# Optimization experiments

Hardware: AMD Instinct MI355X
Metric: run time of the kernel (lower is better)

The kernel has to match this reference:

```python
import jax, jax.numpy as jnp
import numpy as np

BETA = 0.25


def setup_inputs() -> dict:
    key = jax.random.key(0)
    k1, k2 = jax.random.split(key)
    B, C, H, W = 32, 64, 64, 64
    K = 1024
    z = jax.random.normal(k1, (B, C, H, W), dtype=jnp.float32)
    # nn.Embedding init: uniform(-1/K, 1/K)
    embedding = jax.random.uniform(k2, (K, C), dtype=jnp.float32,
                                   minval=-1.0 / K, maxval=1.0 / K)
    return {"z": z, "embedding": embedding}


def reference(z, embedding):
    B, C, H, W = z.shape
    z_hw_c = jnp.transpose(z, (0, 2, 3, 1))            # [B,H,W,C]
    z_flat = z_hw_c.reshape(-1, C)                      # [N,C], N=B*H*W
    # squared L2 distance: ||z||^2 + ||e||^2 - 2 z e^T
    d = (jnp.sum(z_flat ** 2, axis=1, keepdims=True)
         + jnp.sum(embedding ** 2, axis=1)
         - 2.0 * jnp.matmul(z_flat, embedding.T))       # [N,K]
    idx = jnp.argmin(d, axis=1)                         # [N]
    z_q = embedding[idx].reshape(z_hw_c.shape)          # [B,H,W,C]
    # commitment + codebook loss (detach emulated with stop_gradient)
    loss = (jnp.mean((jax.lax.stop_gradient(z_q) - z_hw_c) ** 2)
            + BETA * jnp.mean((z_q - jax.lax.stop_gradient(z_hw_c)) ** 2))
    # straight-through estimator
    z_q_st = z_hw_c + jax.lax.stop_gradient(z_q - z_hw_c)
    z_q_out = jnp.transpose(z_q_st, (0, 3, 1, 2))       # [B,C,H,W]
    min_encoding_indices = idx.reshape(B, H, W)
    return z_q_out, min_encoding_indices, loss
```

## Files before the change

### kernel.cpp

```cpp
#include <hip/hip_runtime.h>

#define C 64
#define K 1024
#define HW 4096
#define N_TOTAL 131072
#define OUT0 8388608
#define MT 128
#define KT 64
#define NTILES (K / KT)

#define WS_EK        0
#define WS_PARTIALS  1024
#define WS_ETG       3072
#define WS_NEED_FLOATS (3072 + C * K)

typedef unsigned int u32;
typedef unsigned long long u64;

__device__ __forceinline__ u64 packdk(float d, int k) {
    u32 b = __float_as_uint(d);
    u32 m = b ^ ((u32)((int)b >> 31) | 0x80000000u);
    return ((u64)m << 32) | (u32)k;
}

__global__ __launch_bounds__(256) void eprep_kernel(const float* __restrict__ E,
                                                    float* __restrict__ Etg,
                                                    float* __restrict__ ek) {
#pragma clang fp contract(off)
    int k = blockIdx.x * 256 + threadIdx.x;
    const float* e = E + k * C;
    float ev[C];
#pragma unroll
    for (int c4 = 0; c4 < 16; ++c4) {
        float4 v = *(const float4*)(e + c4 * 4);
        ev[c4 * 4 + 0] = v.x; ev[c4 * 4 + 1] = v.y;
        ev[c4 * 4 + 2] = v.z; ev[c4 * 4 + 3] = v.w;
    }
    float r[8];
#pragma unroll
    for (int j = 0; j < 8; ++j) r[j] = ev[j] * ev[j];
#pragma unroll
    for (int i = 8; i < C; i += 8)
#pragma unroll
        for (int j = 0; j < 8; ++j) r[j] += ev[i + j] * ev[i + j];
    ek[k] = ((r[0] + r[1]) + (r[2] + r[3])) + ((r[4] + r[5]) + (r[6] + r[7]));
#pragma unroll
    for (int c = 0; c < C; ++c) Etg[c * K + k] = ev[c];
}

__global__ __launch_bounds__(256, 2) void vq_main(const float* __restrict__ Z,
                                                  const float* __restrict__ E,
                                                  const float* __restrict__ Etg,
                                                  const float* __restrict__ ek,
                                                  float* __restrict__ out,
                                                  float* __restrict__ partials) {
#pragma clang fp contract(off)
    __shared__ float Zt[C * MT];
    __shared__ float EtS[C * KT];
    __shared__ float znbuf[MT];
    __shared__ u64 red[4][8][8];

    const int t = threadIdx.x;
    const int n0 = blockIdx.x * MT;
    const int b = n0 >> 12;
    const int hw0 = n0 & 4095;
    const float* zbase = Z + b * (C * HW) + hw0;

#pragma unroll
    for (int r = 0; r < 8; ++r) {
        int idx4 = r * 256 + t;
        int c = idx4 >> 5, n4 = idx4 & 31;
        float4 v = *(const float4*)(zbase + c * HW + n4 * 4);
        *(float4*)(&Zt[c * MT + n4 * 4]) = v;
    }
    __syncthreads();

    if (t < MT) {
        float r8[8];
#pragma unroll
        for (int j = 0; j < 8; ++j) { float v = Zt[j * MT + t]; r8[j] = v * v; }
#pragma unroll
        for (int i = 1; i < 8; ++i)
#pragma unroll
            for (int j = 0; j < 8; ++j) { float v = Zt[(i * 8 + j) * MT + t]; r8[j] += v * v; }
        znbuf[t] = ((r8[0] + r8[1]) + (r8[2] + r8[3])) + ((r8[4] + r8[5]) + (r8[6] + r8[7]));
    }
    __syncthreads();

    const int wave = t >> 6, lane = t & 63;
    const int i_l = lane & 7, j_l = lane >> 3;
    const int ig = ((wave & 1) << 3) | i_l;
    const int jg = ((wave >> 1) << 3) | j_l;

    float znm[8];
#pragma unroll
    for (int m = 0; m < 8; ++m) znm[m] = znbuf[ig * 8 + m];

    float dmin[8];
    int qb[8];
#pragma unroll
    for (int m = 0; m < 8; ++m) { dmin[m] = __builtin_inff(); qb[m] = 0; }

#pragma unroll 1
    for (int tile = 0; tile < NTILES; ++tile) {
        __syncthreads();
#pragma unroll
        for (int p = 0; p < 4; ++p) {
            int idx = p * 256 + t;
            int c = idx >> 4, kk = idx & 15;
            float4 v = *(const float4*)(Etg + c * K + tile * KT + kk * 4);
            *(float4*)(&EtS[c * KT + kk * 4]) = v;
        }
        __syncthreads();

        float4 ekv = *(const float4*)(ek + tile * KT + jg * 4);
        float ekq[4] = {ekv.x, ekv.y, ekv.z, ekv.w};

        float acc[8][4];
#pragma unroll
        for (int m = 0; m < 8; ++m)
#pragma unroll
            for (int q = 0; q < 4; ++q) acc[m][q] = 0.0f;

#pragma unroll 4
        for (int c = 0; c < C; ++c) {
            float4 za = *(const float4*)(&Zt[c * MT + ig * 8]);
            float4 zb = *(const float4*)(&Zt[c * MT + ig * 8 + 4]);
            float4 ea = *(const float4*)(&EtS[c * KT + jg * 4]);
            float zm[8] = {za.x, za.y, za.z, za.w, zb.x, zb.y, zb.z, zb.w};
            float eq[4] = {ea.x, ea.y, ea.z, ea.w};
#pragma unroll
            for (int m = 0; m < 8; ++m)
#pragma unroll
                for (int q = 0; q < 4; ++q)
                    acc[m][q] = __builtin_fmaf(zm[m], eq[q], acc[m][q]);
        }

        const int qbase = tile * 4;
#pragma unroll
        for (int m = 0; m < 8; ++m)
#pragma unroll
            for (int q = 0; q < 4; ++q) {
                float A = znm[m] + ekq[q];
                float d = __builtin_fmaf(-2.0f, acc[m][q], A);
                if (d < dmin[m]) { dmin[m] = d; qb[m] = qbase + q; }
            }
    }

    u64 bestp[8];
#pragma unroll
    for (int m = 0; m < 8; ++m) {
        int q4 = qb[m];
        int k = (q4 >> 2) * KT + jg * 4 + (q4 & 3);
        bestp[m] = packdk(dmin[m], k);
    }
#pragma unroll
    for (int m = 0; m < 8; ++m) {
        u64 v = bestp[m];
#pragma unroll
        for (int mask = 8; mask <= 32; mask <<= 1) {
            u64 o = __shfl_xor(v, mask, 64);
            v = o < v ? o : v;
        }
        bestp[m] = v;
    }
    if (j_l == 0) {
#pragma unroll
        for (int m = 0; m < 8; ++m) red[wave][i_l][m] = bestp[m];
    }
    __syncthreads();

    if (t < MT) {
        int igg = t >> 3, m = t & 7;
        int ihalf = igg >> 3, iw = igg & 7;
        u64 a = red[ihalf][iw][m];
        u64 b2 = red[ihalf + 2][iw][m];
        u64 v = b2 < a ? b2 : a;
        int best = (int)(v & 0xFFFFFFFFu);
        int n = n0 + t;
        out[OUT0 + n] = (float)best;

        const float4* eb4 = (const float4*)(E + best * C);
        float* o0 = out + b * (C * HW) + hw0 + t;
        float ls = 0.0f;
#pragma unroll
        for (int c4 = 0; c4 < 16; ++c4) {
            float4 e4 = eb4[c4];
            int cb = c4 * 4;
            float z0 = Zt[(cb + 0) * MT + t], z1 = Zt[(cb + 1) * MT + t];
            float z2 = Zt[(cb + 2) * MT + t], z3 = Zt[(cb + 3) * MT + t];
            float f0 = e4.x - z0; o0[(cb + 0) * HW] = z0 + f0; ls += f0 * f0;
            float f1 = e4.y - z1; o0[(cb + 1) * HW] = z1 + f1; ls += f1 * f1;
            float f2 = e4.z - z2; o0[(cb + 2) * HW] = z2 + f2; ls += f2 * f2;
            float f3 = e4.w - z3; o0[(cb + 3) * HW] = z3 + f3; ls += f3 * f3;
        }
#pragma unroll
        for (int off = 32; off > 0; off >>= 1) ls += __shfl_xor(ls, off, 64);
        if ((t & 63) == 0) partials[n >> 6] = ls;
    }
}

__global__ __launch_bounds__(256) void ek_kernel(const float* __restrict__ E,
                                                 float* __restrict__ ek) {
#pragma clang fp contract(off)
    int k = blockIdx.x * 256 + threadIdx.x;
    if (k >= K) return;
    const float* e = E + k * C;
    float r[8];
#pragma unroll
    for (int j = 0; j < 8; ++j) { float v = e[j]; r[j] = v * v; }
#pragma unroll
    for (int i = 8; i < C; i += 8) {
#pragma unroll
        for (int j = 0; j < 8; ++j) { float v = e[i + j]; r[j] += v * v; }
    }
    ek[k] = ((r[0] + r[1]) + (r[2] + r[3])) + ((r[4] + r[5]) + (r[6] + r[7]));
}

__global__ __launch_bounds__(256, 4) void vq_combined(const float* __restrict__ Z,
                                                      const float* __restrict__ E,
                                                      const float* __restrict__ ek,
                                                      float* __restrict__ out,
                                                      float* __restrict__ partials) {
#pragma clang fp contract(off)
    int n = blockIdx.x * 256 + threadIdx.x;
    int b = n >> 12;
    int hw = n & 4095;
    const float* zp = Z + b * (C * HW) + hw;

    float z[C];
#pragma unroll
    for (int c = 0; c < C; ++c) z[c] = zp[c * HW];
    float zn;
    {
        float r[8];
#pragma unroll
        for (int j = 0; j < 8; ++j) r[j] = z[j] * z[j];
#pragma unroll
        for (int i = 8; i < C; i += 8) {
#pragma unroll
            for (int j = 0; j < 8; ++j) r[j] += z[i + j] * z[i + j];
        }
        zn = ((r[0] + r[1]) + (r[2] + r[3])) + ((r[4] + r[5]) + (r[6] + r[7]));
    }

    float dmin = __builtin_inff();
    int best = 0;
#pragma unroll 1
    for (int k = 0; k < K; k += 4) {
        const float* e0 = E + k * C;
        float a0 = 0.0f, a1 = 0.0f, a2 = 0.0f, a3 = 0.0f;
#pragma unroll
        for (int c = 0; c < C; ++c) {
            float zc = z[c];
            a0 = __builtin_fmaf(zc, e0[c], a0);
            a1 = __builtin_fmaf(zc, e0[C + c], a1);
            a2 = __builtin_fmaf(zc, e0[2 * C + c], a2);
            a3 = __builtin_fmaf(zc, e0[3 * C + c], a3);
        }
        float A0 = zn + ek[k],     A1 = zn + ek[k + 1];
        float A2 = zn + ek[k + 2], A3 = zn + ek[k + 3];
        float d0 = A0 - 2.0f * a0, d1 = A1 - 2.0f * a1;
        float d2 = A2 - 2.0f * a2, d3 = A3 - 2.0f * a3;
        if (d0 < dmin) { dmin = d0; best = k; }
        if (d1 < dmin) { dmin = d1; best = k + 1; }
        if (d2 < dmin) { dmin = d2; best = k + 2; }
        if (d3 < dmin) { dmin = d3; best = k + 3; }
    }

    const float4* eb4 = (const float4*)(E + best * C);
    float* o0 = out + b * (C * HW) + hw;
    float ls = 0.0f;
#pragma unroll
    for (int c4 = 0; c4 < 16; ++c4) {
        float4 e4 = eb4[c4];
        int cb = c4 * 4;
        float f0 = e4.x - z[cb + 0]; o0[(cb + 0) * HW] = z[cb + 0] + f0; ls += f0 * f0;
        float f1 = e4.y - z[cb + 1]; o0[(cb + 1) * HW] = z[cb + 1] + f1; ls += f1 * f1;
        float f2 = e4.z - z[cb + 2]; o0[(cb + 2) * HW] = z[cb + 2] + f2; ls += f2 * f2;
        float f3 = e4.w - z[cb + 3]; o0[(cb + 3) * HW] = z[cb + 3] + f3; ls += f3 * f3;
    }
    out[OUT0 + n] = (float)best;
#pragma unroll
    for (int off = 32; off > 0; off >>= 1) ls += __shfl_xor(ls, off, 64);
    if ((threadIdx.x & 63) == 0) partials[n >> 6] = ls;
}

__global__ __launch_bounds__(256) void loss_kernel(const float* __restrict__ partials,
                                                   float* __restrict__ out) {
    __shared__ double sm[256];
    int t = threadIdx.x;
    double s = 0.0;
    for (int i = t; i < (N_TOTAL / 64); i += 256) s += (double)partials[i];
    sm[t] = s;
    __syncthreads();
    for (int o = 128; o > 0; o >>= 1) {
        if (t < o) sm[t] += sm[t + o];
        __syncthreads();
    }
    if (t == 0) {
        float m = (float)(sm[0] * (1.0 / 8388608.0));
        float loss = m + 0.25f * m;
        out[OUT0 + N_TOTAL] = loss;
    }
}

extern "C" void kernel_launch(void* const* d_in, const int* in_sizes, int n_in,
                              void* d_out, int out_size, void* d_ws, size_t ws_size,
                              hipStream_t stream) {
    const float* Z = (const float*)d_in[0];
    const float* E = (const float*)d_in[1];
    float* out = (float*)d_out;
    float* ws = (float*)d_ws;
    float* ek = ws + WS_EK;
    float* partials = ws + WS_PARTIALS;

    if (ws_size >= (size_t)WS_NEED_FLOATS * sizeof(float)) {
        float* Etg = ws + WS_ETG;
        hipLaunchKernelGGL(eprep_kernel, dim3(K / 256), dim3(256), 0, stream,
                           E, Etg, ek);
        hipLaunchKernelGGL(vq_main, dim3(N_TOTAL / MT), dim3(256), 0, stream,
                           Z, E, Etg, ek, out, partials);
    } else {
        hipLaunchKernelGGL(ek_kernel, dim3(4), dim3(256), 0, stream, E, ek);
        hipLaunchKernelGGL(vq_combined, dim3(N_TOTAL / 256), dim3(256), 0, stream,
                           Z, E, ek, out, partials);
    }
    hipLaunchKernelGGL(loss_kernel, dim3(1), dim3(256), 0, stream, partials, out);
}
```

Measured before the change: 234.4 us.

## Compute VQ distances with split-bf16 MFMA plus exact fp32 fallback for ambiguous rows

Replaces the scalar fp32 FMA distance GEMM with bf16 hi/lo split MFMA (3-term product) over a pre-swizzled bf16 codebook loaded to LDS via global_load_lds. Each row tracks best and second-best distance; rows with a small gap (or a failed spot check against an fp32 dot) are appended to a list and recomputed exactly in fp32 by a fallback kernel. The epilogue and loss are split into separate kernels. The intent is to move the dominant matmul onto matrix cores, at the cost of extra launches, a second pass over Z, and atomics.

```diff
diff --git a/kernel.cpp b/kernel.cpp
--- a/kernel.cpp
+++ b/kernel.cpp
@@ -6,27 +6,47 @@
 #define N_TOTAL 131072
 #define OUT0 8388608
 #define MT 128
-#define KT 64
-#define NTILES (K / KT)
+#define KT2 64
+#define NT2 (K / KT2)
+
+#define GAP_THR 2.5e-4f
+#define CHK_THR 1e-4f
 
 #define WS_EK        0
-#define WS_PARTIALS  1024
-#define WS_ETG       3072
-#define WS_NEED_FLOATS (3072 + C * K)
+#define WS_ROWLOSS   1024
+#define WS_BESTI     132096
+#define WS_ULIST     263168
+#define WS_UCOUNT    394240
+#define WS_EBF       394256
+#define WS_NEED2     (394256 + 32768)
 
 typedef unsigned int u32;
 typedef unsigned long long u64;
+typedef __attribute__((ext_vector_type(8))) short short8;
+typedef __attribute__((ext_vector_type(4))) float f32x4;
+typedef const __attribute__((address_space(1))) void* gas_ptr;
+typedef __attribute__((address_space(3))) void* las_ptr;
 
 __device__ __forceinline__ u64 packdk(float d, int k) {
     u32 b = __float_as_uint(d);
     u32 m = b ^ ((u32)((int)b >> 31) | 0x80000000u);
     return ((u64)m << 32) | (u32)k;
 }
-
-__global__ __launch_bounds__(256) void eprep_kernel(const float* __restrict__ E,
-                                                    float* __restrict__ Etg,
-                                                    float* __restrict__ ek) {
-#pragma clang fp contract(off)
+__device__ __forceinline__ unsigned short f2bf(float x) {
+    u32 u = __float_as_uint(x);
+    return (unsigned short)((u + 0x7FFFu + ((u >> 16) & 1u)) >> 16);
+}
+__device__ __forceinline__ float bf2f(unsigned short h) {
+    u32 u = ((u32)h) << 16;
+    return __uint_as_float(u);
+}
+
+__global__ __launch_bounds__(256) void eprep2(const float* __restrict__ E,
+                                              float* __restrict__ ek,
+                                              short* __restrict__ EbfS,
+                                              int* __restrict__ ucount) {
+#pragma clang fp contract(off)
+    if (blockIdx.x == 0 && threadIdx.x == 0) *ucount = 0;
     int k = blockIdx.x * 256 + threadIdx.x;
     const float* e = E + k * C;
     float ev[C];
@@ -44,159 +64,278 @@
 #pragma unroll
         for (int j = 0; j < 8; ++j) r[j] += ev[i + j] * ev[i + j];
     ek[k] = ((r[0] + r[1]) + (r[2] + r[3])) + ((r[4] + r[5]) + (r[6] + r[7]));
-#pragma unroll
-    for (int c = 0; c < C; ++c) Etg[c * K + k] = ev[c];
-}
-
-__global__ __launch_bounds__(256, 2) void vq_main(const float* __restrict__ Z,
-                                                  const float* __restrict__ E,
-                                                  const float* __restrict__ Etg,
+
+    unsigned short hi[C], lo[C];
+#pragma unroll
+    for (int c = 0; c < C; ++c) {
+        unsigned short h = f2bf(ev[c]);
+        hi[c] = h;
+        lo[c] = f2bf(ev[c] - bf2f(h));
+    }
+#pragma unroll
+    for (int ci = 0; ci < 16; ++ci) {
+        int p = ci >> 3, c0 = (ci & 7) * 8;
+        short8 v;
+#pragma unroll
+        for (int e2 = 0; e2 < 8; ++e2)
+            v[e2] = (short)(p ? lo[c0 + e2] : hi[c0 + e2]);
+        int slot = k * 16 + (ci ^ (k & 7));
+        *(short8*)&EbfS[slot * 8] = v;
+    }
+}
+
+__global__ __launch_bounds__(256, 2) void vq_mfma(const float* __restrict__ Z,
+                                                  const float* __restrict__ Efp,
                                                   const float* __restrict__ ek,
-                                                  float* __restrict__ out,
-                                                  float* __restrict__ partials) {
-#pragma clang fp contract(off)
-    __shared__ float Zt[C * MT];
-    __shared__ float EtS[C * KT];
-    __shared__ float znbuf[MT];
-    __shared__ u64 red[4][8][8];
+                                                  const short* __restrict__ EbfS,
+                                                  int* __restrict__ besti,
+                                                  int* __restrict__ ulist,
+                                                  int* __restrict__ ucount) {
+#pragma clang fp contract(off)
+    __shared__ float SA[8192];
+    __shared__ unsigned short Zb[16384];
+    __shared__ int flagLds;
 
     const int t = threadIdx.x;
+    const int wave = t >> 6, lane = t & 63;
     const int n0 = blockIdx.x * MT;
     const int b = n0 >> 12;
     const int hw0 = n0 & 4095;
     const float* zbase = Z + b * (C * HW) + hw0;
+    if (t == 0) flagLds = 0;
 
 #pragma unroll
     for (int r = 0; r < 8; ++r) {
         int idx4 = r * 256 + t;
         int c = idx4 >> 5, n4 = idx4 & 31;
         float4 v = *(const float4*)(zbase + c * HW + n4 * 4);
-        *(float4*)(&Zt[c * MT + n4 * 4]) = v;
+        *(float4*)(&SA[c * MT + n4 * 4]) = v;
     }
     __syncthreads();
 
-    if (t < MT) {
-        float r8[8];
-#pragma unroll
-        for (int j = 0; j < 8; ++j) { float v = Zt[j * MT + t]; r8[j] = v * v; }
-#pragma unroll
-        for (int i = 1; i < 8; ++i)
-#pragma unroll
-            for (int j = 0; j < 8; ++j) { float v = Zt[(i * 8 + j) * MT + t]; r8[j] += v * v; }
-        znbuf[t] = ((r8[0] + r8[1]) + (r8[2] + r8[3])) + ((r8[4] + r8[5]) + (r8[6] + r8[7]));
+    const int wr = wave * 32;
+    float a_chk = 0.0f;
+    {
+        int rl = wr + ((lane >> 4) << 2);
+        const float* ep = Efp + (lane & 15) * C;
+#pragma unroll 4
+        for (int c = 0; c < C; ++c)
+            a_chk = __builtin_fmaf(SA[c * MT + rl], ep[c], a_chk);
+    }
+    {
+        int r = t & 127, p = t >> 7;
+#pragma unroll
+        for (int c8 = 0; c8 < 8; ++c8) {
+            short8 v;
+#pragma unroll
+            for (int e2 = 0; e2 < 8; ++e2) {
+                float z = SA[(c8 * 8 + e2) * MT + r];
+                unsigned short h = f2bf(z);
+                v[e2] = (short)(p ? f2bf(z - bf2f(h)) : h);
+            }
+            *(short8*)&Zb[r * 128 + p * 64 + c8 * 8] = v;
+        }
     }
     __syncthreads();
 
-    const int wave = t >> 6, lane = t & 63;
-    const int i_l = lane & 7, j_l = lane >> 3;
-    const int ig = ((wave & 1) << 3) | i_l;
-    const int jg = ((wave >> 1) << 3) | j_l;
-
-    float znm[8];
-#pragma unroll
-    for (int m = 0; m < 8; ++m) znm[m] = znbuf[ig * 8 + m];
-
-    float dmin[8];
-    int qb[8];
-#pragma unroll
-    for (int m = 0; m < 8; ++m) { dmin[m] = __builtin_inff(); qb[m] = 0; }
+    short8 af[2][2][2];
+#pragma unroll
+    for (int rt = 0; rt < 2; ++rt)
+#pragma unroll
+        for (int ks = 0; ks < 2; ++ks)
+#pragma unroll
+            for (int p = 0; p < 2; ++p)
+                af[rt][ks][p] = *(const short8*)&Zb[(wr + rt * 16 + (lane & 15)) * 128
+                                                   + p * 64 + ks * 32 + ((lane >> 4) << 3)];
+
+#pragma unroll
+    for (int p2 = 0; p2 < 4; ++p2) {
+        int q = wave * 4 + p2;
+        const char* gsrc = (const char*)EbfS + q * 1024 + lane * 16;
+        __builtin_amdgcn_global_load_lds((gas_ptr)gsrc,
+                                         (las_ptr)((char*)SA + q * 1024), 16, 0, 0);
+    }
+    __syncthreads();
+
+    float d1f[8], d2f[8];
+    int k1[8];
+#pragma unroll
+    for (int s = 0; s < 8; ++s) { d1f[s] = __builtin_inff(); d2f[s] = __builtin_inff(); k1[s] = 0; }
 
 #pragma unroll 1
-    for (int tile = 0; tile < NTILES; ++tile) {
+    for (int tau = 0; tau < NT2; ++tau) {
+#pragma unroll 1
+        for (int cg = 0; cg < 4; ++cg) {
+            int kl = cg * 16 + (lane & 15);
+            int kg = tau * KT2 + kl;
+            float ekv = ek[kg];
+            short8 bf_[2][2];
+#pragma unroll
+            for (int ks = 0; ks < 2; ++ks)
+#pragma unroll
+                for (int p = 0; p < 2; ++p) {
+                    int ci = p * 8 + ks * 4 + (lane >> 4);
+                    int sca = kl * 16 + (ci ^ (kl & 7));
+                    bf_[ks][p] = *(const short8*)((const char*)SA + sca * 16);
+                }
+#pragma unroll
+            for (int rt = 0; rt < 2; ++rt) {
+                f32x4 acc = {0.0f, 0.0f, 0.0f, 0.0f};
+                acc = __builtin_amdgcn_mfma_f32_16x16x32_bf16(af[rt][0][0], bf_[0][0], acc, 0, 0, 0);
+                acc = __builtin_amdgcn_mfma_f32_16x16x32_bf16(af[rt][0][0], bf_[0][1], acc, 0, 0, 0);
+                acc = __builtin_amdgcn_mfma_f32_16x16x32_bf16(af[rt][0][1], bf_[0][0], acc, 0, 0, 0);
+                acc = __builtin_amdgcn_mfma_f32_16x16x32_bf16(af[rt][1][0], bf_[1][0], acc, 0, 0, 0);
+                acc = __builtin_amdgcn_mfma_f32_16x16x32_bf16(af[rt][1][0], bf_[1][1], acc, 0, 0, 0);
+                acc = __builtin_amdgcn_mfma_f32_16x16x32_bf16(af[rt][1][1], bf_[1][0], acc, 0, 0, 0);
+                if (tau == 0 && cg == 0 && rt == 0) {
+                    if (__builtin_fabsf(acc[0] - a_chk) > CHK_THR) flagLds = 1;
+                }
+#pragma unroll
+                for (int j = 0; j < 4; ++j) {
+                    float d = __builtin_fmaf(-2.0f, acc[j], ekv);
+                    int s = rt * 4 + j;
+                    if (d < d1f[s]) { d2f[s] = d1f[s]; d1f[s] = d; k1[s] = kg; }
+                    else if (d < d2f[s]) { d2f[s] = d; }
+                }
+            }
+        }
         __syncthreads();
-#pragma unroll
-        for (int p = 0; p < 4; ++p) {
-            int idx = p * 256 + t;
-            int c = idx >> 4, kk = idx & 15;
-            float4 v = *(const float4*)(Etg + c * K + tile * KT + kk * 4);
-            *(float4*)(&EtS[c * KT + kk * 4]) = v;
+        if (tau + 1 < NT2) {
+#pragma unroll
+            for (int p2 = 0; p2 < 4; ++p2) {
+                int q = wave * 4 + p2;
+                const char* gsrc = (const char*)EbfS + (tau + 1) * 16384 + q * 1024 + lane * 16;
+                __builtin_amdgcn_global_load_lds((gas_ptr)gsrc,
+                                                 (las_ptr)((char*)SA + q * 1024), 16, 0, 0);
+            }
         }
         __syncthreads();
-
-        float4 ekv = *(const float4*)(ek + tile * KT + jg * 4);
-        float ekq[4] = {ekv.x, ekv.y, ekv.z, ekv.w};
-
-        float acc[8][4];
-#pragma unroll
-        for (int m = 0; m < 8; ++m)
-#pragma unroll
-            for (int q = 0; q < 4; ++q) acc[m][q] = 0.0f;
-
-#pragma unroll 4
-        for (int c = 0; c < C; ++c) {
-            float4 za = *(const float4*)(&Zt[c * MT + ig * 8]);
-            float4 zb = *(const float4*)(&Zt[c * MT + ig * 8 + 4]);
-            float4 ea = *(const float4*)(&EtS[c * KT + jg * 4]);
-            float zm[8] = {za.x, za.y, za.z, za.w, zb.x, zb.y, zb.z, zb.w};
-            float eq[4] = {ea.x, ea.y, ea.z, ea.w};
-#pragma unroll
-            for (int m = 0; m < 8; ++m)
-#pragma unroll
-                for (int q = 0; q < 4; ++q)
-                    acc[m][q] = __builtin_fmaf(zm[m], eq[q], acc[m][q]);
-        }
-
-        const int qbase = tile * 4;
-#pragma unroll
-        for (int m = 0; m < 8; ++m)
-#pragma unroll
-            for (int q = 0; q < 4; ++q) {
-                float A = znm[m] + ekq[q];
-                float d = __builtin_fmaf(-2.0f, acc[m][q], A);
-                if (d < dmin[m]) { dmin[m] = d; qb[m] = qbase + q; }
+    }
+
+#pragma unroll
+    for (int s = 0; s < 8; ++s) {
+        u64 pk = packdk(d1f[s], k1[s]);
+        float d1 = d1f[s], d2 = d2f[s];
+#pragma unroll
+        for (int m = 1; m <= 8; m <<= 1) {
+            u64 po = __shfl_xor(pk, m, 64);
+            float d1o = __shfl_xor(d1, m, 64);
+            float d2o = __shfl_xor(d2, m, 64);
+            d2 = fminf(fminf(d2, d2o), fmaxf(d1, d1o));
+            d1 = fminf(d1, d1o);
+            pk = po < pk ? po : pk;
+        }
+        d1f[s] = d1; d2f[s] = d2; k1[s] = (int)(pk & 0xFFFFFFFFull);
+    }
+    int flg = flagLds;
+    if ((lane & 15) == 0) {
+#pragma unroll
+        for (int s = 0; s < 8; ++s) {
+            int rt = s >> 2, j = s & 3;
+            int n = n0 + wr + rt * 16 + ((lane >> 4) << 2) + j;
+            besti[n] = k1[s];
+            float gap = d2f[s] - d1f[s];
+            if (flg || !(gap > GAP_THR)) {
+                int ix = atomicAdd(ucount, 1);
+                ulist[ix] = n;
             }
-    }
-
-    u64 bestp[8];
-#pragma unroll
-    for (int m = 0; m < 8; ++m) {
-        int q4 = qb[m];
-        int k = (q4 >> 2) * KT + jg * 4 + (q4 & 3);
-        bestp[m] = packdk(dmin[m], k);
-    }
-#pragma unroll
-    for (int m = 0; m < 8; ++m) {
-        u64 v = bestp[m];
-#pragma unroll
-        for (int mask = 8; mask <= 32; mask <<= 1) {
-            u64 o = __shfl_xor(v, mask, 64);
-            v = o < v ? o : v;
-        }
-        bestp[m] = v;
-    }
-    if (j_l == 0) {
-#pragma unroll
-        for (int m = 0; m < 8; ++m) red[wave][i_l][m] = bestp[m];
-    }
+        }
+    }
+}
+
+__global__ __launch_bounds__(256) void vq_fallback(const float* __restrict__ Z,
+                                                   const float* __restrict__ E,
+                                                   const float* __restrict__ ek,
+                                                   const int* __restrict__ ulist,
+                                                   const int* __restrict__ ucount,
+                                                   int* __restrict__ besti) {
+#pragma clang fp contract(off)
+    int wid = blockIdx.x * 4 + (threadIdx.x >> 6);
+    int lane = threadIdx.x & 63;
+    int cnt = *ucount;
+    for (int i = wid; i < cnt; i += gridDim.x * 4) {
+        int n = ulist[i];
+        int b = n >> 12, hw = n & 4095;
+        const float* zp = Z + b * (C * HW) + hw;
+        float zr[C];
+#pragma unroll
+        for (int c = 0; c < C; ++c) zr[c] = zp[c * HW];
+        float zn;
+        {
+            float r[8];
+#pragma unroll
+            for (int j = 0; j < 8; ++j) r[j] = zr[j] * zr[j];
+#pragma unroll
+            for (int q = 8; q < C; q += 8)
+#pragma unroll
+                for (int j = 0; j < 8; ++j) r[j] += zr[q + j] * zr[q + j];
+            zn = ((r[0] + r[1]) + (r[2] + r[3])) + ((r[4] + r[5]) + (r[6] + r[7]));
+        }
+        u64 best = ~0ull;
+#pragma unroll 1
+        for (int j = 0; j < 16; ++j) {
+            int k = j * 64 + lane;
+            const float* e = E + k * C;
+            float a = 0.0f;
+#pragma unroll
+            for (int c = 0; c < C; ++c) a = __builtin_fmaf(zr[c], e[c], a);
+            float A = zn + ek[k];
+            float d = A - 2.0f * a;
+            u64 p = packdk(d, k);
+            if (p < best) best = p;
+        }
+#pragma unroll
+        for (int m = 1; m <= 32; m <<= 1) {
+            u64 o = __shfl_xor(best, m, 64);
+            best = o < best ? o : best;
+        }
+        if (lane == 0) besti[n] = (int)(best & 0xFFFFFFFFull);
+    }
+}
+
+__global__ __launch_bounds__(256) void vq_epilogue2(const float* __restrict__ Z,
+                                                    const float* __restrict__ E,
+                                                    const int* __restrict__ besti,
+                                                    float* __restrict__ out,
+                                                    float* __restrict__ rowloss) {
+#pragma clang fp contract(off)
+    int n = blockIdx.x * 256 + threadIdx.x;
+    int b = n >> 12, hw = n & 4095;
+    int best = besti[n];
+    const float* zp = Z + b * (C * HW) + hw;
+    const float4* eb4 = (const float4*)(E + best * C);
+    float* o0 = out + b * (C * HW) + hw;
+    float ls = 0.0f;
+#pragma unroll
+    for (int c4 = 0; c4 < 16; ++c4) {
+        float4 e4 = eb4[c4];
+        int cb = c4 * 4;
+        float z0 = zp[(cb + 0) * HW], z1 = zp[(cb + 1) * HW];
+        float z2 = zp[(cb + 2) * HW], z3 = zp[(cb + 3) * HW];
+        float f0 = e4.x - z0; o0[(cb + 0) * HW] = z0 + f0; ls += f0 * f0;
+        float f1 = e4.y - z1; o0[(cb + 1) * HW] = z1 + f1; ls += f1 * f1;
+        float f2 = e4.z - z2; o0[(cb + 2) * HW] = z2 + f2; ls += f2 * f2;
+        float f3 = e4.w - z3; o0[(cb + 3) * HW] = z3 + f3; ls += f3 * f3;
+    }
+    out[OUT0 + n] = (float)best;
+    rowloss[n] = ls;
+}
+
+__global__ __launch_bounds__(256) void loss2(const float* __restrict__ rowloss,
+                                             float* __restrict__ out) {
+    __shared__ double sm[256];
+    int t = threadIdx.x;
+    double s = 0.0;
+    for (int i = t; i < N_TOTAL; i += 256) s += (double)rowloss[i];
+    sm[t] = s;
     __syncthreads();
-
-    if (t < MT) {
-        int igg = t >> 3, m = t & 7;
-        int ihalf = igg >> 3, iw = igg & 7;
-        u64 a = red[ihalf][iw][m];
-        u64 b2 = red[ihalf + 2][iw][m];
-        u64 v = b2 < a ? b2 : a;
-        int best = (int)(v & 0xFFFFFFFFu);
-        int n = n0 + t;
-        out[OUT0 + n] = (float)best;
-
-        const float4* eb4 = (const float4*)(E + best * C);
-        float* o0 = out + b * (C * HW) + hw0 + t;
-        float ls = 0.0f;
-#pragma unroll
-        for (int c4 = 0; c4 < 16; ++c4) {
-            float4 e4 = eb4[c4];
-            int cb = c4 * 4;
-            float z0 = Zt[(cb + 0) * MT + t], z1 = Zt[(cb + 1) * MT + t];
-            float z2 = Zt[(cb + 2) * MT + t], z3 = Zt[(cb + 3) * MT + t];
-            float f0 = e4.x - z0; o0[(cb + 0) * HW] = z0 + f0; ls += f0 * f0;
-            float f1 = e4.y - z1; o0[(cb + 1) * HW] = z1 + f1; ls += f1 * f1;
-            float f2 = e4.z - z2; o0[(cb + 2) * HW] = z2 + f2; ls += f2 * f2;
-            float f3 = e4.w - z3; o0[(cb + 3) * HW] = z3 + f3; ls += f3 * f3;
-        }
-#pragma unroll
-        for (int off = 32; off > 0; off >>= 1) ls += __shfl_xor(ls, off, 64);
-        if ((t & 63) == 0) partials[n >> 6] = ls;
+    for (int o = 128; o > 0; o >>= 1) {
+        if (t < o) sm[t] += sm[t + o];
+        __syncthreads();
+    }
+    if (t == 0) {
+        float m = (float)(sm[0] * (1.0 / 8388608.0));
+        out[OUT0 + N_TOTAL] = m + 0.25f * m;
     }
 }
 
@@ -210,10 +349,9 @@
 #pragma unroll
     for (int j = 0; j < 8; ++j) { float v = e[j]; r[j] = v * v; }
 #pragma unroll
-    for (int i = 8; i < C; i += 8) {
+    for (int i = 8; i < C; i += 8)
 #pragma unroll
         for (int j = 0; j < 8; ++j) { float v = e[i + j]; r[j] += v * v; }
-    }
     ek[k] = ((r[0] + r[1]) + (r[2] + r[3])) + ((r[4] + r[5]) + (r[6] + r[7]));
 }
 
@@ -224,10 +362,8 @@
                                                       float* __restrict__ partials) {
 #pragma clang fp contract(off)
     int n = blockIdx.x * 256 + threadIdx.x;
-    int b = n >> 12;
-    int hw = n & 4095;
+    int b = n >> 12, hw = n & 4095;
     const float* zp = Z + b * (C * HW) + hw;
-
     float z[C];
 #pragma unroll
     for (int c = 0; c < C; ++c) z[c] = zp[c * HW];
@@ -237,13 +373,11 @@
 #pragma unroll
         for (int j = 0; j < 8; ++j) r[j] = z[j] * z[j];
 #pragma unroll
-        for (int i = 8; i < C; i += 8) {
+        for (int i = 8; i < C; i += 8)
 #pragma unroll
             for (int j = 0; j < 8; ++j) r[j] += z[i + j] * z[i + j];
-        }
         zn = ((r[0] + r[1]) + (r[2] + r[3])) + ((r[4] + r[5]) + (r[6] + r[7]));
     }
-
     float dmin = __builtin_inff();
     int best = 0;
 #pragma unroll 1
@@ -267,7 +401,6 @@
         if (d2 < dmin) { dmin = d2; best = k + 2; }
         if (d3 < dmin) { dmin = d3; best = k + 3; }
     }
-
     const float4* eb4 = (const float4*)(E + best * C);
     float* o0 = out + b * (C * HW) + hw;
     float ls = 0.0f;
@@ -300,8 +433,7 @@
     }
     if (t == 0) {
         float m = (float)(sm[0] * (1.0 / 8388608.0));
-        float loss = m + 0.25f * m;
-        out[OUT0 + N_TOTAL] = loss;
+        out[OUT0 + N_TOTAL] = m + 0.25f * m;
     }
 }
 
@@ -313,18 +445,28 @@
     float* out = (float*)d_out;
     float* ws = (float*)d_ws;
     float* ek = ws + WS_EK;
-    float* partials = ws + WS_PARTIALS;
-
-    if (ws_size >= (size_t)WS_NEED_FLOATS * sizeof(float)) {
-        float* Etg = ws + WS_ETG;
-        hipLaunchKernelGGL(eprep_kernel, dim3(K / 256), dim3(256), 0, stream,
-                           E, Etg, ek);
-        hipLaunchKernelGGL(vq_main, dim3(N_TOTAL / MT), dim3(256), 0, stream,
-                           Z, E, Etg, ek, out, partials);
+
+    if (ws_size >= (size_t)WS_NEED2 * sizeof(float)) {
+        float* rowloss = ws + WS_ROWLOSS;
+        int* besti  = (int*)(ws + WS_BESTI);
+        int* ulist  = (int*)(ws + WS_ULIST);
+        int* ucount = (int*)(ws + WS_UCOUNT);
+        short* EbfS = (short*)(ws + WS_EBF);
+
+        hipLaunchKernelGGL(eprep2, dim3(K / 256), dim3(256), 0, stream,
+                           E, ek, EbfS, ucount);
+        hipLaunchKernelGGL(vq_mfma, dim3(N_TOTAL / MT), dim3(256), 0, stream,
+                           Z, E, ek, EbfS, besti, ulist, ucount);
+        hipLaunchKernelGGL(vq_fallback, dim3(1024), dim3(256), 0, stream,
+                           Z, E, ek, ulist, ucount, besti);
+        hipLaunchKernelGGL(vq_epilogue2, dim3(N_TOTAL / 256), dim3(256), 0, stream,
+                           Z, E, besti, out, rowloss);
+        hipLaunchKernelGGL(loss2, dim3(1), dim3(256), 0, stream, rowloss, out);
     } else {
+        float* partials = ws + 1024;
         hipLaunchKernelGGL(ek_kernel, dim3(4), dim3(256), 0, stream, E, ek);
         hipLaunchKernelGGL(vq_combined, dim3(N_TOTAL / 256), dim3(256), 0, stream,
                            Z, E, ek, out, partials);
-    }
-    hipLaunchKernelGGL(loss_kernel, dim3(1), dim3(256), 0, stream, partials, out);
-}
+        hipLaunchKernelGGL(loss_kernel, dim3(1), dim3(256), 0, stream, partials, out);
+    }
+}
```

Result: slower. 753.5 us (+221.4%).
